# Optimization experiments

Measured on AMD Instinct MI355X. Metric: run time of the kernel, lower is better.

## Reference

```python
import jax, jax.numpy as jnp
import numpy as np

B, T, D, H = 4, 1024, 1024, 16
DH = D // H
EPS = 1e-5


def setup_inputs() -> dict:
    key = jax.random.key(0)
    ks = jax.random.split(key, 14)
    sc = 1.0 / np.sqrt(D)
    x = jax.random.normal(ks[0], (B, T, D), jnp.float32)
    W_r = jax.random.normal(ks[1], (D, D), jnp.float32) * sc
    W_k = jax.random.normal(ks[2], (D, D), jnp.float32) * sc
    W_v = jax.random.normal(ks[3], (D, D), jnp.float32) * sc
    W_w = jax.random.normal(ks[4], (D, D), jnp.float32) * sc
    W_o = jax.random.normal(ks[5], (D, D), jnp.float32) * sc
    u = jax.random.normal(ks[6], (H, DH), jnp.float32) * 0.1
    tm_r = jax.random.uniform(ks[7], (D,), jnp.float32)
    tm_k = jax.random.uniform(ks[8], (D,), jnp.float32)
    tm_v = jax.random.uniform(ks[9], (D,), jnp.float32)
    tm_w = jax.random.uniform(ks[10], (D,), jnp.float32)
    ln_w = jnp.ones((DH,), jnp.float32) + 0.1 * jax.random.normal(ks[11], (DH,), jnp.float32)
    ln_b = 0.1 * jax.random.normal(ks[12], (DH,), jnp.float32)
    return {"x": x, "W_r": W_r, "W_k": W_k, "W_v": W_v, "W_w": W_w, "W_o": W_o,
            "u": u, "tm_r": tm_r, "tm_k": tm_k, "tm_v": tm_v, "tm_w": tm_w,
            "ln_w": ln_w, "ln_b": ln_b}


def _rwkv6(x, W_r, W_k, W_v, W_w, W_o, u, tm_r, tm_k, tm_v, tm_w, ln_w, ln_b):
    b, t, d = x.shape
    # token-shift mix
    x_prev = jnp.concatenate([jnp.zeros_like(x[:, :1]), x[:, :-1]], axis=1)
    xr = tm_r * x + (1.0 - tm_r) * x_prev
    xk = tm_k * x + (1.0 - tm_k) * x_prev
    xv = tm_v * x + (1.0 - tm_v) * x_prev
    xw = tm_w * x + (1.0 - tm_w) * x_prev
    r = jax.nn.sigmoid(xr @ W_r.T)          # (B,T,D)
    k = xk @ W_k.T
    v = xv @ W_v.T
    w = -jax.nn.softplus(-(xw @ W_w.T)) - 1e-4  # always < 0 -> exp(w) in (0,1)
    r = r.reshape(b, t, H, DH)
    k = k.reshape(b, t, H, DH)
    v = v.reshape(b, t, H, DH)
    w = w.reshape(b, t, H, DH)

    def step(s, rkvw):
        r_t, k_t, v_t, w_t = rkvw  # each (B,H,DH)
        bonus = jnp.exp(u + k_t)[..., :, None] * v_t[..., None, :]  # (B,H,DH,DH)
        o_t = jnp.einsum('bhi,bhij->bhj', r_t, s + bonus)
        s = jnp.exp(w_t)[..., None] * s + k_t[..., :, None] * v_t[..., None, :]
        return s, o_t

    s0 = jnp.zeros((b, H, DH, DH), x.dtype)
    rkvw = tuple(a.transpose(1, 0, 2, 3) for a in (r, k, v, w))  # (T,B,H,DH)
    _, o = jax.lax.scan(step, s0, rkvw)      # o: (T,B,H,DH)
    o = o.transpose(1, 0, 2, 3)              # (B,T,H,DH)
    # group LayerNorm over head dim
    mu = jnp.mean(o, axis=-1, keepdims=True)
    var = jnp.var(o, axis=-1, keepdims=True)
    o = (o - mu) * jax.lax.rsqrt(var + EPS) * ln_w + ln_b
    o = o * r
    return (o.reshape(b, t, d)) @ W_o.T


def reference(x, W_r, W_k, W_v, W_w, W_o, u, tm_r, tm_k, tm_v, tm_w, ln_w, ln_b):
    return _rwkv6(x, W_r, W_k, W_v, W_w, W_o, u, tm_r, tm_k, tm_v, tm_w, ln_w, ln_b)
```

## Files before the change

### kernel.cpp

```cpp
#include <hip/hip_runtime.h>


typedef unsigned short u16;
typedef unsigned int   u32;

typedef __attribute__((ext_vector_type(8))) __bf16 bf16x8;
typedef __attribute__((ext_vector_type(4))) float   f32x4;

#define MB (1u << 20)

#define LDS_PTR(p) ((__attribute__((address_space(3))) void*)(p))
#define GLB_PTR(p) ((const __attribute__((address_space(1))) void*)(p))

__device__ __forceinline__ u16 f2bf(float f) {
  u32 u = __builtin_bit_cast(u32, f);
  u += 0x7FFFu + ((u >> 16) & 1u);
  return (u16)(u >> 16);
}
__device__ __forceinline__ float bf2f(u16 x) {
  u32 u = ((u32)x) << 16;
  return __builtin_bit_cast(float, u);
}
__device__ __forceinline__ u32 pack2(float a, float b) {
  return (u32)f2bf(a) | ((u32)f2bf(b) << 16);
}

__global__ __launch_bounds__(256) void prep_w(
    const float* __restrict__ w0, const float* __restrict__ w1,
    const float* __restrict__ w2, const float* __restrict__ w3,
    const float* __restrict__ w4, u32* __restrict__ out) {
  int idx = blockIdx.x * 256 + threadIdx.x;
  int m = idx >> 19;
  int l = idx & 524287;
  const float* src = (m == 0) ? w0 : (m == 1) ? w1 : (m == 2) ? w2 : (m == 3) ? w3 : w4;
  float2 v = *(const float2*)(src + (size_t)l * 2);
  out[idx] = pack2(v.x, v.y);
}

__global__ __launch_bounds__(256) void prep_mix(
    const float* __restrict__ x,
    const float* __restrict__ tmr, const float* __restrict__ tmk,
    const float* __restrict__ tmv, const float* __restrict__ tmw,
    u32* __restrict__ xr, u32* __restrict__ xk,
    u32* __restrict__ xv, u32* __restrict__ xw) {
  int idx = blockIdx.x * 256 + threadIdx.x;
  int t  = (idx >> 9) & 1023;
  int d0 = (idx & 511) * 2;
  size_t e = (size_t)idx * 2;
  float2 xc = *(const float2*)(x + e);
  float2 xp = make_float2(0.f, 0.f);
  if (t > 0) xp = *(const float2*)(x + e - 1024);
  float2 tm;
  tm = *(const float2*)(tmr + d0);
  xr[idx] = pack2(tm.x * xc.x + (1.f - tm.x) * xp.x, tm.y * xc.y + (1.f - tm.y) * xp.y);
  tm = *(const float2*)(tmk + d0);
  xk[idx] = pack2(tm.x * xc.x + (1.f - tm.x) * xp.x, tm.y * xc.y + (1.f - tm.y) * xp.y);
  tm = *(const float2*)(tmv + d0);
  xv[idx] = pack2(tm.x * xc.x + (1.f - tm.x) * xp.x, tm.y * xc.y + (1.f - tm.y) * xp.y);
  tm = *(const float2*)(tmw + d0);
  xw[idx] = pack2(tm.x * xc.x + (1.f - tm.x) * xp.x, tm.y * xc.y + (1.f - tm.y) * xp.y);
}

__global__ __launch_bounds__(512, 1) void gemm_proj(
    const u16* __restrict__ xr, const u16* __restrict__ xk,
    const u16* __restrict__ xv, const u16* __restrict__ xw,
    const u16* __restrict__ Wr, const u16* __restrict__ Wk,
    const u16* __restrict__ Wv, const u16* __restrict__ Ww,
    u16* __restrict__ rO, u16* __restrict__ kO,
    u16* __restrict__ vO, float* __restrict__ wO) {
  constexpr int KITER = 16;
  constexpr int LDK   = 1024;
  __shared__ __align__(16) u16 Asm[2 * 16384];
  __shared__ __align__(16) u16 Bsm[2 * 16384];

  int mat = blockIdx.z;
  const u16* A = (mat == 0) ? xr : (mat == 1) ? xk : (mat == 2) ? xv : xw;
  const u16* W = (mat == 0) ? Wr : (mat == 1) ? Wk : (mat == 2) ? Wv : Ww;

  int tid = threadIdx.x;
  int m0 = blockIdx.x * 256, n0 = blockIdx.y * 256;
  int wave = tid >> 6, lane = tid & 63;
  int wm = (wave >> 2) * 128;
  int wn = (wave & 3) * 64;
  int r16 = lane & 15, quad = lane >> 4;

  f32x4 acc[8][4] = {};

  int lrow  = lane >> 3;
  int lchk  = (lane & 7) ^ lrow;
  const u16* Ag[4];
  const u16* Bg[4];
#pragma unroll
  for (int i = 0; i < 4; ++i) {
    int row = wave * 32 + i * 8 + lrow;
    Ag[i] = A + (size_t)(m0 + row) * LDK + lchk * 8;
    Bg[i] = W + (size_t)(n0 + row) * LDK + lchk * 8;
  }
  int ldsW = wave * 2048;

  int aoff[8], boff[4];
#pragma unroll
  for (int mt = 0; mt < 8; ++mt) {
    int r = wm + mt * 16 + r16;
    aoff[mt] = r * 64 + (quad ^ (r16 & 7)) * 8;
  }
#pragma unroll
  for (int nt = 0; nt < 4; ++nt) {
    int r = wn + nt * 16 + r16;
    boff[nt] = r * 64 + (quad ^ (r16 & 7)) * 8;
  }

#define ISSUE_TILE(t, buf)                                                              \
  do {                                                                                  \
    int _o = (buf) * 16384 + ldsW, _k = (t) * 64;                                       \
    __builtin_amdgcn_global_load_lds(GLB_PTR(Ag[0] + _k), LDS_PTR(Asm + _o),        16, 0, 0); \
    __builtin_amdgcn_global_load_lds(GLB_PTR(Ag[1] + _k), LDS_PTR(Asm + _o + 512),  16, 0, 0); \
    __builtin_amdgcn_global_load_lds(GLB_PTR(Ag[2] + _k), LDS_PTR(Asm + _o + 1024), 16, 0, 0); \
    __builtin_amdgcn_global_load_lds(GLB_PTR(Ag[3] + _k), LDS_PTR(Asm + _o + 1536), 16, 0, 0); \
    __builtin_amdgcn_global_load_lds(GLB_PTR(Bg[0] + _k), LDS_PTR(Bsm + _o),        16, 0, 0); \
    __builtin_amdgcn_global_load_lds(GLB_PTR(Bg[1] + _k), LDS_PTR(Bsm + _o + 512),  16, 0, 0); \
    __builtin_amdgcn_global_load_lds(GLB_PTR(Bg[2] + _k), LDS_PTR(Bsm + _o + 1024), 16, 0, 0); \
    __builtin_amdgcn_global_load_lds(GLB_PTR(Bg[3] + _k), LDS_PTR(Bsm + _o + 1536), 16, 0, 0); \
  } while (0)

  ISSUE_TILE(0, 0);
  ISSUE_TILE(1, 1);

  int cur = 0;
  for (int i = 0; i < KITER; ++i) {
    if (i < KITER - 1) asm volatile("s_waitcnt vmcnt(8)" ::: "memory");
    else               asm volatile("s_waitcnt vmcnt(0)" ::: "memory");
    __builtin_amdgcn_s_barrier();

    const u16* As = Asm + cur * 16384;
    const u16* Bs = Bsm + cur * 16384;
#pragma unroll
    for (int kk = 0; kk < 2; ++kk) {
      int kx = kk * 32;
      bf16x8 af[8], bfm[4];
#pragma unroll
      for (int mt = 0; mt < 8; ++mt) af[mt] = *(const bf16x8*)&As[aoff[mt] ^ kx];
#pragma unroll
      for (int nt = 0; nt < 4; ++nt) bfm[nt] = *(const bf16x8*)&Bs[boff[nt] ^ kx];
#pragma unroll
      for (int mt = 0; mt < 8; ++mt)
#pragma unroll
        for (int nt = 0; nt < 4; ++nt)
          acc[mt][nt] = __builtin_amdgcn_mfma_f32_16x16x32_bf16(af[mt], bfm[nt], acc[mt][nt], 0, 0, 0);
    }

    asm volatile("s_waitcnt lgkmcnt(0)" ::: "memory");
    __builtin_amdgcn_s_barrier();
    if (i + 2 < KITER) ISSUE_TILE(i + 2, cur);
    cur ^= 1;
  }
#undef ISSUE_TILE

#pragma unroll
  for (int mt = 0; mt < 8; ++mt) {
#pragma unroll
    for (int nt = 0; nt < 4; ++nt) {
#pragma unroll
      for (int rg = 0; rg < 4; ++rg) {
        int row = m0 + wm + mt * 16 + quad * 4 + rg;
        int col = n0 + wn + nt * 16 + r16;
        float v = acc[mt][nt][rg];
        size_t idx = (size_t)row * 1024 + col;
        if (mat == 0)      rO[idx] = f2bf(1.f / (1.f + __expf(-v)));
        else if (mat == 1) kO[idx] = f2bf(v);
        else if (mat == 2) vO[idx] = f2bf(v);
        else               wO[idx] = v;
      }
    }
  }
}

__global__ __launch_bounds__(512, 1) void gemm_out_ks(
    const u16* __restrict__ A0, const u16* __restrict__ W0,
    float* __restrict__ P0, float* __restrict__ P1,
    float* __restrict__ P2, float* __restrict__ P3) {
  constexpr int KITER = 4;
  constexpr int LDK   = 1024;
  __shared__ __align__(16) u16 Asm[2 * 16384];
  __shared__ __align__(16) u16 Bsm[2 * 16384];

  int z = blockIdx.z;
  const u16* A = A0 + z * 256;
  const u16* W = W0 + z * 256;
  float* P = (z == 0) ? P0 : (z == 1) ? P1 : (z == 2) ? P2 : P3;

  int tid = threadIdx.x;
  int m0 = blockIdx.x * 256, n0 = blockIdx.y * 256;
  int wave = tid >> 6, lane = tid & 63;
  int wm = (wave >> 2) * 128;
  int wn = (wave & 3) * 64;
  int r16 = lane & 15, quad = lane >> 4;

  f32x4 acc[8][4] = {};

  int lrow  = lane >> 3;
  int lchk  = (lane & 7) ^ lrow;
  const u16* Ag[4];
  const u16* Bg[4];
#pragma unroll
  for (int i = 0; i < 4; ++i) {
    int row = wave * 32 + i * 8 + lrow;
    Ag[i] = A + (size_t)(m0 + row) * LDK + lchk * 8;
    Bg[i] = W + (size_t)(n0 + row) * LDK + lchk * 8;
  }
  int ldsW = wave * 2048;

  int aoff[8], boff[4];
#pragma unroll
  for (int mt = 0; mt < 8; ++mt) {
    int r = wm + mt * 16 + r16;
    aoff[mt] = r * 64 + (quad ^ (r16 & 7)) * 8;
  }
#pragma unroll
  for (int nt = 0; nt < 4; ++nt) {
    int r = wn + nt * 16 + r16;
    boff[nt] = r * 64 + (quad ^ (r16 & 7)) * 8;
  }

#define ISSUE_TILE(t, buf)                                                              \
  do {                                                                                  \
    int _o = (buf) * 16384 + ldsW, _k = (t) * 64;                                       \
    __builtin_amdgcn_global_load_lds(GLB_PTR(Ag[0] + _k), LDS_PTR(Asm + _o),        16, 0, 0); \
    __builtin_amdgcn_global_load_lds(GLB_PTR(Ag[1] + _k), LDS_PTR(Asm + _o + 512),  16, 0, 0); \
    __builtin_amdgcn_global_load_lds(GLB_PTR(Ag[2] + _k), LDS_PTR(Asm + _o + 1024), 16, 0, 0); \
    __builtin_amdgcn_global_load_lds(GLB_PTR(Ag[3] + _k), LDS_PTR(Asm + _o + 1536), 16, 0, 0); \
    __builtin_amdgcn_global_load_lds(GLB_PTR(Bg[0] + _k), LDS_PTR(Bsm + _o),        16, 0, 0); \
    __builtin_amdgcn_global_load_lds(GLB_PTR(Bg[1] + _k), LDS_PTR(Bsm + _o + 512),  16, 0, 0); \
    __builtin_amdgcn_global_load_lds(GLB_PTR(Bg[2] + _k), LDS_PTR(Bsm + _o + 1024), 16, 0, 0); \
    __builtin_amdgcn_global_load_lds(GLB_PTR(Bg[3] + _k), LDS_PTR(Bsm + _o + 1536), 16, 0, 0); \
  } while (0)

  ISSUE_TILE(0, 0);
  ISSUE_TILE(1, 1);

  int cur = 0;
  for (int i = 0; i < KITER; ++i) {
    if (i < KITER - 1) asm volatile("s_waitcnt vmcnt(8)" ::: "memory");
    else               asm volatile("s_waitcnt vmcnt(0)" ::: "memory");
    __builtin_amdgcn_s_barrier();

    const u16* As = Asm + cur * 16384;
    const u16* Bs = Bsm + cur * 16384;
#pragma unroll
    for (int kk = 0; kk < 2; ++kk) {
      int kx = kk * 32;
      bf16x8 af[8], bfm[4];
#pragma unroll
      for (int mt = 0; mt < 8; ++mt) af[mt] = *(const bf16x8*)&As[aoff[mt] ^ kx];
#pragma unroll
      for (int nt = 0; nt < 4; ++nt) bfm[nt] = *(const bf16x8*)&Bs[boff[nt] ^ kx];
#pragma unroll
      for (int mt = 0; mt < 8; ++mt)
#pragma unroll
        for (int nt = 0; nt < 4; ++nt)
          acc[mt][nt] = __builtin_amdgcn_mfma_f32_16x16x32_bf16(af[mt], bfm[nt], acc[mt][nt], 0, 0, 0);
    }

    asm volatile("s_waitcnt lgkmcnt(0)" ::: "memory");
    __builtin_amdgcn_s_barrier();
    if (i + 2 < KITER) ISSUE_TILE(i + 2, cur);
    cur ^= 1;
  }
#undef ISSUE_TILE

#pragma unroll
  for (int mt = 0; mt < 8; ++mt)
#pragma unroll
    for (int nt = 0; nt < 4; ++nt)
#pragma unroll
      for (int rg = 0; rg < 4; ++rg) {
        int row = m0 + wm + mt * 16 + quad * 4 + rg;
        int col = n0 + wn + nt * 16 + r16;
        P[(size_t)row * 1024 + col] = acc[mt][nt][rg];
      }
}

__global__ __launch_bounds__(256) void reduce_out(
    const float4* __restrict__ p0, const float4* __restrict__ p1,
    const float4* __restrict__ p2, const float4* __restrict__ p3,
    float4* __restrict__ out) {
  int i = blockIdx.x * 256 + threadIdx.x;
  float4 a = p0[i], b = p1[i], c = p2[i], d = p3[i];
  out[i] = make_float4(a.x + b.x + c.x + d.x, a.y + b.y + c.y + d.y,
                       a.z + b.z + c.z + d.z, a.w + b.w + c.w + d.w);
}

__global__ __launch_bounds__(256) void scan_intra(
    const u16* __restrict__ rb, const u16* __restrict__ kb,
    const u16* __restrict__ vb, const float* __restrict__ wb,
    const float* __restrict__ u,
    float* __restrict__ o, u16* __restrict__ rd,
    float* __restrict__ U, float* __restrict__ Dc) {
  int c = blockIdx.x, bh = blockIdx.y;
  int b = bh >> 4, h = bh & 15;
  int tid = threadIdx.x;
  int wave = tid >> 6, lane = tid & 63;
  int ig4 = tid >> 4, jq = tid & 15;

  __shared__ __align__(16) float4 combo[4][64];
  __shared__ __align__(16) float4 vs4[4][16];
  __shared__ __align__(16) float  part[4][16][68];

  const float EW_SCALE = 0.99990001f;

  float s[4][4];
#pragma unroll
  for (int ii = 0; ii < 4; ++ii)
#pragma unroll
    for (int jj = 0; jj < 4; ++jj) s[ii][jj] = 0.f;

  size_t base = ((size_t)(b * 1024 + c * 32)) * 1024 + h * 64 + lane;
  float dloc = 1.0f;
  float uval = (wave < 2) ? u[h * 64 + lane] : 0.f;

#define STAGE(t2, sl)                                                     \
  do {                                                                    \
    size_t _idx = base + (size_t)(t2) * 1024;                             \
    if (wave < 2) {                                                       \
      float _r = bf2f(rb[_idx]);                                          \
      float _k = bf2f(kb[_idx]);                                          \
      float _z = wb[_idx];                                                \
      combo[sl][lane] = make_float4(_r, _k, __expf(uval + _k),            \
                                    EW_SCALE / (1.f + __expf(-_z)));      \
    } else {                                                              \
      ((float*)vs4)[(sl) * 64 + lane] = bf2f(vb[_idx]);                   \
    }                                                                     \
  } while (0)

  { int p = wave & 1; STAGE(p, p); }
  __syncthreads();

  for (int tt = 0; tt < 32; tt += 2) {
    if (tt + 2 < 32) {
      int p = wave & 1;
      int t2 = tt + 2 + p;
      STAGE(t2, t2 & 3);
    }
#pragma unroll
    for (int p = 0; p < 2; ++p) {
      int t = tt + p, sl = t & 3;
      float4 vv = vs4[sl][jq];
      float4 cb0 = combo[sl][ig4 * 4 + 0];
      float4 cb1 = combo[sl][ig4 * 4 + 1];
      float4 cb2 = combo[sl][ig4 * 4 + 2];
      float4 cb3 = combo[sl][ig4 * 4 + 3];
      float ac0 = 0.f, ac1 = 0.f, ac2 = 0.f, ac3 = 0.f;
#define ROW(cb, ii)                                                       \
      do {                                                                \
        float t0 = fmaf(cb.z, vv.x, s[ii][0]);                            \
        float t1 = fmaf(cb.z, vv.y, s[ii][1]);                            \
        float t2_ = fmaf(cb.z, vv.z, s[ii][2]);                           \
        float t3 = fmaf(cb.z, vv.w, s[ii][3]);                            \
        ac0 = fmaf(cb.x, t0, ac0);                                        \
        ac1 = fmaf(cb.x, t1, ac1);                                        \
        ac2 = fmaf(cb.x, t2_, ac2);                                       \
        ac3 = fmaf(cb.x, t3, ac3);                                        \
        s[ii][0] = fmaf(cb.w, s[ii][0], cb.y * vv.x);                     \
        s[ii][1] = fmaf(cb.w, s[ii][1], cb.y * vv.y);                     \
        s[ii][2] = fmaf(cb.w, s[ii][2], cb.y * vv.z);                     \
        s[ii][3] = fmaf(cb.w, s[ii][3], cb.y * vv.w);                     \
      } while (0)
      ROW(cb0, 0); ROW(cb1, 1); ROW(cb2, 2); ROW(cb3, 3);
#undef ROW
      *(float4*)&part[sl][ig4][jq * 4] = make_float4(ac0, ac1, ac2, ac3);
      if (wave == 0) {
        float4 me = combo[sl][lane];
        rd[base + (size_t)t * 1024] = f2bf(me.x * dloc);
        dloc *= me.w;
      }
    }
    if (tt >= 2) {
      if (wave == 2) {
        int t = tt - 2, sl = t & 3;
        float sum = 0.f;
#pragma unroll
        for (int g = 0; g < 16; ++g) sum += part[sl][g][lane];
        o[base + (size_t)t * 1024] = sum;
      } else if (wave == 3) {
        int t = tt - 1, sl = t & 3;
        float sum = 0.f;
#pragma unroll
        for (int g = 0; g < 16; ++g) sum += part[sl][g][lane];
        o[base + (size_t)t * 1024] = sum;
      }
    }
    __syncthreads();
  }
#undef STAGE
  if (wave == 2) {
    float sum = 0.f;
#pragma unroll
    for (int g = 0; g < 16; ++g) sum += part[2][g][lane];
    o[base + (size_t)30 * 1024] = sum;
  } else if (wave == 3) {
    float sum = 0.f;
#pragma unroll
    for (int g = 0; g < 16; ++g) sum += part[3][g][lane];
    o[base + (size_t)31 * 1024] = sum;
  }

  float* Ug = U + (size_t)(bh * 32 + c) * 4096;
#pragma unroll
  for (int ii = 0; ii < 4; ++ii) {
    *(float4*)&Ug[(ig4 * 4 + ii) * 64 + jq * 4] =
        make_float4(s[ii][0], s[ii][1], s[ii][2], s[ii][3]);
  }
  if (wave == 0) Dc[(bh * 32 + c) * 64 + lane] = dloc;
}

__global__ __launch_bounds__(256) void state_prop(
    float* __restrict__ U, const float* __restrict__ Dc) {
  int bh  = blockIdx.x >> 4;
  int e   = (blockIdx.x & 15) * 256 + threadIdx.x;
  int i   = e >> 6;
  float acc = 0.f;
  for (int c = 0; c < 32; ++c) {
    float* Ug = U + (size_t)(bh * 32 + c) * 4096 + e;
    float d = Dc[(bh * 32 + c) * 64 + i];
    float uv = *Ug;
    *Ug = acc;
    acc = fmaf(d, acc, uv);
  }
}

__global__ __launch_bounds__(128) void inter_ln(
    const float* __restrict__ o, const u16* __restrict__ rd,
    const u16* __restrict__ rb, const float* __restrict__ U,
    const float* __restrict__ lnw, const float* __restrict__ lnb,
    u16* __restrict__ oh) {
  int c = blockIdx.x, bh = blockIdx.y;
  int b = bh >> 4, h = bh & 15;
  int tid = threadIdx.x, wave = tid >> 6, lane = tid & 63;
  int l15 = lane & 15, quad = lane >> 4;

  __shared__ __align__(16) u16 Sb[64][72];

  const float* Sg = U + (size_t)(bh * 32 + c) * 4096;
#pragma unroll
  for (int q = 0; q < 32; ++q) {
    int e = q * 128 + tid;
    Sb[e & 63][e >> 6] = f2bf(Sg[e]);
  }
  __syncthreads();

  size_t rbase = ((size_t)(b * 1024 + c * 32)) * 1024 + h * 64;

  const u16* rdg = rd + rbase + (size_t)(wave * 16 + l15) * 1024 + quad * 8;
  bf16x8 af0 = *(const bf16x8*)(rdg);
  bf16x8 af1 = *(const bf16x8*)(rdg + 32);

  f32x4 acc[4] = {};
#pragma unroll
  for (int nt = 0; nt < 4; ++nt) {
    const u16* bp = &Sb[nt * 16 + l15][quad * 8];
    bf16x8 b0 = *(const bf16x8*)bp;
    bf16x8 b1 = *(const bf16x8*)(bp + 32);
    acc[nt] = __builtin_amdgcn_mfma_f32_16x16x32_bf16(af0, b0, acc[nt], 0, 0, 0);
    acc[nt] = __builtin_amdgcn_mfma_f32_16x16x32_bf16(af1, b1, acc[nt], 0, 0, 0);
  }

#pragma unroll
  for (int rg = 0; rg < 4; ++rg) {
    int t = wave * 16 + quad * 4 + rg;
    size_t rowb = rbase + (size_t)t * 1024;
    float v[4];
    float s1 = 0.f, s2 = 0.f;
#pragma unroll
    for (int nt = 0; nt < 4; ++nt) {
      v[nt] = acc[nt][rg] + o[rowb + nt * 16 + l15];
      s1 += v[nt];
      s2 += v[nt] * v[nt];
    }
#pragma unroll
    for (int m = 1; m < 16; m <<= 1) {
      s1 += __shfl_xor(s1, m, 64);
      s2 += __shfl_xor(s2, m, 64);
    }
    float mu  = s1 * (1.f / 64.f);
    float var = s2 * (1.f / 64.f) - mu * mu;
    float rstd = rsqrtf(var + 1e-5f);
#pragma unroll
    for (int nt = 0; nt < 4; ++nt) {
      int jj = nt * 16 + l15;
      float nv = (v[nt] - mu) * rstd;
      float val = (nv * lnw[jj] + lnb[jj]) * bf2f(rb[rowb + jj]);
      oh[rowb + jj] = f2bf(val);
    }
  }
}

extern "C" void kernel_launch(void* const* d_in, const int* in_sizes, int n_in,
                              void* d_out, int out_size, void* d_ws, size_t ws_size,
                              hipStream_t stream) {
  const float* x    = (const float*)d_in[0];
  const float* W_r  = (const float*)d_in[1];
  const float* W_k  = (const float*)d_in[2];
  const float* W_v  = (const float*)d_in[3];
  const float* W_w  = (const float*)d_in[4];
  const float* W_o  = (const float*)d_in[5];
  const float* u    = (const float*)d_in[6];
  const float* tm_r = (const float*)d_in[7];
  const float* tm_k = (const float*)d_in[8];
  const float* tm_v = (const float*)d_in[9];
  const float* tm_w = (const float*)d_in[10];
  const float* ln_w = (const float*)d_in[11];
  const float* ln_b = (const float*)d_in[12];
  float* out = (float*)d_out;

  char* ws = (char*)d_ws;
  u16* xr = (u16*)(ws + (size_t)0 * MB);
  u16* xk = (u16*)(ws + (size_t)8 * MB);
  u16* xv = (u16*)(ws + (size_t)16 * MB);
  u16* xw = (u16*)(ws + (size_t)24 * MB);
  float* Ubuf = (float*)(ws + (size_t)0 * MB);
  u16* Wb = (u16*)(ws + (size_t)32 * MB);
  u16* Wrb = Wb;
  u16* Wkb = (u16*)(ws + (size_t)34 * MB);
  u16* Wvb = (u16*)(ws + (size_t)36 * MB);
  u16* Wwb = (u16*)(ws + (size_t)38 * MB);
  u16* Wob = (u16*)(ws + (size_t)40 * MB);
  float* Dcbuf = (float*)(ws + (size_t)42 * MB);
  u16*   rbuf = (u16*)(ws + (size_t)48 * MB);
  u16*   kbuf = (u16*)(ws + (size_t)56 * MB);
  u16*   vbuf = (u16*)(ws + (size_t)64 * MB);
  float* wbuf = (float*)(ws + (size_t)72 * MB);
  float* obuf = (float*)(ws + (size_t)88 * MB);
  u16*  rdbuf = (u16*)(ws + (size_t)104 * MB);
  u16*   ohbuf = (u16*)(ws + (size_t)129 * MB);
  float* P0 = (float*)(ws + (size_t)48 * MB);
  float* P1 = (float*)(ws + (size_t)64 * MB);
  float* P2 = (float*)(ws + (size_t)80 * MB);
  float* P3 = (float*)(ws + (size_t)96 * MB);

  prep_w<<<10240, 256, 0, stream>>>(W_r, W_k, W_v, W_w, W_o, (u32*)Wb);
  prep_mix<<<8192, 256, 0, stream>>>(x, tm_r, tm_k, tm_v, tm_w,
                                     (u32*)xr, (u32*)xk, (u32*)xv, (u32*)xw);
  gemm_proj<<<dim3(16, 4, 4), 512, 0, stream>>>(xr, xk, xv, xw,
                                                Wrb, Wkb, Wvb, Wwb,
                                                rbuf, kbuf, vbuf, wbuf);
  scan_intra<<<dim3(32, 64), 256, 0, stream>>>(rbuf, kbuf, vbuf, wbuf, u,
                                               obuf, rdbuf, Ubuf, Dcbuf);
  state_prop<<<1024, 256, 0, stream>>>(Ubuf, Dcbuf);
  inter_ln<<<dim3(32, 64), 128, 0, stream>>>(obuf, rdbuf, rbuf, Ubuf,
                                             ln_w, ln_b, ohbuf);
  gemm_out_ks<<<dim3(16, 4, 4), 512, 0, stream>>>(ohbuf, Wob, P0, P1, P2, P3);
  reduce_out<<<4096, 256, 0, stream>>>((const float4*)P0, (const float4*)P1,
                                       (const float4*)P2, (const float4*)P3,
                                       (float4*)out);
}
```

Baseline: 254.4 us.

## Replace split-K output GEMM plus reduce kernel with intra-block split-K via LDS

The output projection previously ran a 4-way split-K GEMM over 256x256 tiles, writing four fp32 partial buffers that a separate kernel then summed. It now uses 128x128 tiles on a 32x8 grid. Each block's two 4-wave groups each handle half of K and combine their accumulators through LDS before writing the final output directly. This removes the partial-buffer global traffic and one kernel launch. In exchange, each block does less reuse per tile and the epilogue adds an extra LDS round trip and barrier.

```diff
diff --git a/kernel.cpp b/kernel.cpp
--- a/kernel.cpp
+++ b/kernel.cpp
@@ -175,28 +175,21 @@
   }
 }
 
-__global__ __launch_bounds__(512, 1) void gemm_out_ks(
-    const u16* __restrict__ A0, const u16* __restrict__ W0,
-    float* __restrict__ P0, float* __restrict__ P1,
-    float* __restrict__ P2, float* __restrict__ P3) {
-  constexpr int KITER = 4;
+__global__ __launch_bounds__(512, 1) void gemm_out_sk(
+    const u16* __restrict__ A, const u16* __restrict__ W,
+    float* __restrict__ O) {
+  constexpr int KITER = 8;
   constexpr int LDK   = 1024;
-  __shared__ __align__(16) u16 Asm[2 * 16384];
-  __shared__ __align__(16) u16 Bsm[2 * 16384];
-
-  int z = blockIdx.z;
-  const u16* A = A0 + z * 256;
-  const u16* W = W0 + z * 256;
-  float* P = (z == 0) ? P0 : (z == 1) ? P1 : (z == 2) ? P2 : P3;
+  __shared__ __align__(16) u16 SMEM[2][2][2][8192];
 
   int tid = threadIdx.x;
-  int m0 = blockIdx.x * 256, n0 = blockIdx.y * 256;
+  int m0 = blockIdx.x * 128, n0 = blockIdx.y * 128;
   int wave = tid >> 6, lane = tid & 63;
-  int wm = (wave >> 2) * 128;
-  int wn = (wave & 3) * 64;
+  int grp = wave >> 2, w4 = wave & 3;
+  int wm = (w4 >> 1) * 64, wn = (w4 & 1) * 64;
   int r16 = lane & 15, quad = lane >> 4;
 
-  f32x4 acc[8][4] = {};
+  f32x4 acc[4][4] = {};
 
   int lrow  = lane >> 3;
   int lchk  = (lane & 7) ^ lrow;
@@ -204,15 +197,17 @@
   const u16* Bg[4];
 #pragma unroll
   for (int i = 0; i < 4; ++i) {
-    int row = wave * 32 + i * 8 + lrow;
-    Ag[i] = A + (size_t)(m0 + row) * LDK + lchk * 8;
-    Bg[i] = W + (size_t)(n0 + row) * LDK + lchk * 8;
-  }
-  int ldsW = wave * 2048;
-
-  int aoff[8], boff[4];
-#pragma unroll
-  for (int mt = 0; mt < 8; ++mt) {
+    int row = w4 * 32 + i * 8 + lrow;
+    Ag[i] = A + (size_t)(m0 + row) * LDK + grp * 512 + lchk * 8;
+    Bg[i] = W + (size_t)(n0 + row) * LDK + grp * 512 + lchk * 8;
+  }
+  u16* Abase = &SMEM[0][grp][0][0];
+  u16* Bbase = &SMEM[1][grp][0][0];
+  int ldsW = w4 * 2048;
+
+  int aoff[4], boff[4];
+#pragma unroll
+  for (int mt = 0; mt < 4; ++mt) {
     int r = wm + mt * 16 + r16;
     aoff[mt] = r * 64 + (quad ^ (r16 & 7)) * 8;
   }
@@ -224,15 +219,15 @@
 
 #define ISSUE_TILE(t, buf)                                                              \
   do {                                                                                  \
-    int _o = (buf) * 16384 + ldsW, _k = (t) * 64;                                       \
-    __builtin_amdgcn_global_load_lds(GLB_PTR(Ag[0] + _k), LDS_PTR(Asm + _o),        16, 0, 0); \
-    __builtin_amdgcn_global_load_lds(GLB_PTR(Ag[1] + _k), LDS_PTR(Asm + _o + 512),  16, 0, 0); \
-    __builtin_amdgcn_global_load_lds(GLB_PTR(Ag[2] + _k), LDS_PTR(Asm + _o + 1024), 16, 0, 0); \
-    __builtin_amdgcn_global_load_lds(GLB_PTR(Ag[3] + _k), LDS_PTR(Asm + _o + 1536), 16, 0, 0); \
-    __builtin_amdgcn_global_load_lds(GLB_PTR(Bg[0] + _k), LDS_PTR(Bsm + _o),        16, 0, 0); \
-    __builtin_amdgcn_global_load_lds(GLB_PTR(Bg[1] + _k), LDS_PTR(Bsm + _o + 512),  16, 0, 0); \
-    __builtin_amdgcn_global_load_lds(GLB_PTR(Bg[2] + _k), LDS_PTR(Bsm + _o + 1024), 16, 0, 0); \
-    __builtin_amdgcn_global_load_lds(GLB_PTR(Bg[3] + _k), LDS_PTR(Bsm + _o + 1536), 16, 0, 0); \
+    int _o = (buf) * 8192 + ldsW, _k = (t) * 64;                                        \
+    __builtin_amdgcn_global_load_lds(GLB_PTR(Ag[0] + _k), LDS_PTR(Abase + _o),        16, 0, 0); \
+    __builtin_amdgcn_global_load_lds(GLB_PTR(Ag[1] + _k), LDS_PTR(Abase + _o + 512),  16, 0, 0); \
+    __builtin_amdgcn_global_load_lds(GLB_PTR(Ag[2] + _k), LDS_PTR(Abase + _o + 1024), 16, 0, 0); \
+    __builtin_amdgcn_global_load_lds(GLB_PTR(Ag[3] + _k), LDS_PTR(Abase + _o + 1536), 16, 0, 0); \
+    __builtin_amdgcn_global_load_lds(GLB_PTR(Bg[0] + _k), LDS_PTR(Bbase + _o),        16, 0, 0); \
+    __builtin_amdgcn_global_load_lds(GLB_PTR(Bg[1] + _k), LDS_PTR(Bbase + _o + 512),  16, 0, 0); \
+    __builtin_amdgcn_global_load_lds(GLB_PTR(Bg[2] + _k), LDS_PTR(Bbase + _o + 1024), 16, 0, 0); \
+    __builtin_amdgcn_global_load_lds(GLB_PTR(Bg[3] + _k), LDS_PTR(Bbase + _o + 1536), 16, 0, 0); \
   } while (0)
 
   ISSUE_TILE(0, 0);
@@ -244,18 +239,18 @@
     else               asm volatile("s_waitcnt vmcnt(0)" ::: "memory");
     __builtin_amdgcn_s_barrier();
 
-    const u16* As = Asm + cur * 16384;
-    const u16* Bs = Bsm + cur * 16384;
+    const u16* As = Abase + cur * 8192;
+    const u16* Bs = Bbase + cur * 8192;
 #pragma unroll
     for (int kk = 0; kk < 2; ++kk) {
       int kx = kk * 32;
-      bf16x8 af[8], bfm[4];
-#pragma unroll
-      for (int mt = 0; mt < 8; ++mt) af[mt] = *(const bf16x8*)&As[aoff[mt] ^ kx];
+      bf16x8 af[4], bfm[4];
+#pragma unroll
+      for (int mt = 0; mt < 4; ++mt) af[mt] = *(const bf16x8*)&As[aoff[mt] ^ kx];
 #pragma unroll
       for (int nt = 0; nt < 4; ++nt) bfm[nt] = *(const bf16x8*)&Bs[boff[nt] ^ kx];
 #pragma unroll
-      for (int mt = 0; mt < 8; ++mt)
+      for (int mt = 0; mt < 4; ++mt)
 #pragma unroll
         for (int nt = 0; nt < 4; ++nt)
           acc[mt][nt] = __builtin_amdgcn_mfma_f32_16x16x32_bf16(af[mt], bfm[nt], acc[mt][nt], 0, 0, 0);
@@ -268,26 +263,31 @@
   }
 #undef ISSUE_TILE
 
-#pragma unroll
-  for (int mt = 0; mt < 8; ++mt)
-#pragma unroll
-    for (int nt = 0; nt < 4; ++nt)
-#pragma unroll
-      for (int rg = 0; rg < 4; ++rg) {
-        int row = m0 + wm + mt * 16 + quad * 4 + rg;
-        int col = n0 + wn + nt * 16 + r16;
-        P[(size_t)row * 1024 + col] = acc[mt][nt][rg];
+  float* red = (float*)&SMEM[0][0][0][0];
+  int slot = (tid & 255) * 68;
+  if (grp == 1) {
+#pragma unroll
+    for (int mt = 0; mt < 4; ++mt)
+#pragma unroll
+      for (int nt = 0; nt < 4; ++nt)
+        *(f32x4*)&red[slot + (mt * 4 + nt) * 4] = acc[mt][nt];
+  }
+  __syncthreads();
+  if (grp == 0) {
+#pragma unroll
+    for (int mt = 0; mt < 4; ++mt) {
+#pragma unroll
+      for (int nt = 0; nt < 4; ++nt) {
+        f32x4 other = *(const f32x4*)&red[slot + (mt * 4 + nt) * 4];
+#pragma unroll
+        for (int rg = 0; rg < 4; ++rg) {
+          int row = m0 + wm + mt * 16 + quad * 4 + rg;
+          int col = n0 + wn + nt * 16 + r16;
+          O[(size_t)row * 1024 + col] = acc[mt][nt][rg] + other[rg];
+        }
       }
-}
-
-__global__ __launch_bounds__(256) void reduce_out(
-    const float4* __restrict__ p0, const float4* __restrict__ p1,
-    const float4* __restrict__ p2, const float4* __restrict__ p3,
-    float4* __restrict__ out) {
-  int i = blockIdx.x * 256 + threadIdx.x;
-  float4 a = p0[i], b = p1[i], c = p2[i], d = p3[i];
-  out[i] = make_float4(a.x + b.x + c.x + d.x, a.y + b.y + c.y + d.y,
-                       a.z + b.z + c.z + d.z, a.w + b.w + c.w + d.w);
+    }
+  }
 }
 
 __global__ __launch_bounds__(256) void scan_intra(
@@ -532,10 +532,6 @@
   float* obuf = (float*)(ws + (size_t)88 * MB);
   u16*  rdbuf = (u16*)(ws + (size_t)104 * MB);
   u16*   ohbuf = (u16*)(ws + (size_t)129 * MB);
-  float* P0 = (float*)(ws + (size_t)48 * MB);
-  float* P1 = (float*)(ws + (size_t)64 * MB);
-  float* P2 = (float*)(ws + (size_t)80 * MB);
-  float* P3 = (float*)(ws + (size_t)96 * MB);
 
   prep_w<<<10240, 256, 0, stream>>>(W_r, W_k, W_v, W_w, W_o, (u32*)Wb);
   prep_mix<<<8192, 256, 0, stream>>>(x, tm_r, tm_k, tm_v, tm_w,
@@ -548,8 +544,5 @@
   state_prop<<<1024, 256, 0, stream>>>(Ubuf, Dcbuf);
   inter_ln<<<dim3(32, 64), 128, 0, stream>>>(obuf, rdbuf, rbuf, Ubuf,
                                              ln_w, ln_b, ohbuf);
-  gemm_out_ks<<<dim3(16, 4, 4), 512, 0, stream>>>(ohbuf, Wob, P0, P1, P2, P3);
-  reduce_out<<<4096, 256, 0, stream>>>((const float4*)P0, (const float4*)P1,
-                                       (const float4*)P2, (const float4*)P3,
-                                       (float4*)out);
-}
+  gemm_out_sk<<<dim3(32, 8), 512, 0, stream>>>(ohbuf, Wob, out);
+}
```

Result: faster. 238.8 us (-6.1%).
